# Optimization experiments

Hardware: AMD Instinct MI355X
Metric: run time of the kernel (lower is better)

## Reference

```python
import jax, jax.numpy as jnp
import numpy as np

B, T = 64, 2048
VOCAB, H, OUT = 32000, 256, 256


def setup_inputs() -> dict:
    key = jax.random.key(0)
    ks = jax.random.split(key, 6)
    x = jax.random.randint(ks[0], (B, T), 0, VOCAB, dtype=jnp.int32)
    embed = jax.random.normal(ks[1], (VOCAB, H), dtype=jnp.float32) * 0.02
    # torch Linear(h+h, h): weight [h, 2h]; we store transposed [2h, h]
    W_fc = jax.random.normal(ks[2], (2 * H, H), dtype=jnp.float32) * (1.0 / np.sqrt(2 * H))
    b_fc = jax.random.normal(ks[3], (H,), dtype=jnp.float32) * 0.01
    W_out = jax.random.normal(ks[4], (H, OUT), dtype=jnp.float32) * (1.0 / np.sqrt(H))
    b_out = jax.random.normal(ks[5], (OUT,), dtype=jnp.float32) * 0.01
    return {"x": x, "embed": embed, "W_fc": W_fc, "b_fc": b_fc, "W_out": W_out, "b_out": b_out}


def reference(x, embed, W_fc, b_fc, W_out, b_out):
    # SimpleRNN.forward_bptt: h_t = tanh(fc(concat([embed(x_t), h_{t-1}])))
    # concat-linear split: fc([e, h]) = e @ Wx + h @ Wh + b
    h_dim = embed.shape[1]
    Wx, Wh = W_fc[:h_dim], W_fc[h_dim:]
    xe = embed[x]                                   # [B, T, H] gather
    xproj = jnp.einsum('bth,hk->btk', xe, Wx) + b_fc  # precompute input projection

    def step(h, xp_t):
        h_new = jnp.tanh(xp_t + h @ Wh)
        return h_new, h_new

    h0 = jnp.zeros((x.shape[0], h_dim), dtype=embed.dtype)
    h_last, hs = jax.lax.scan(step, h0, jnp.swapaxes(xproj, 0, 1))  # hs: [T, B, H]
    hs = jnp.swapaxes(hs, 0, 1)                     # [B, T, H] = stack(hs[1:], dim=1)
    out = h_last @ W_out + b_out                    # [B, OUT]
    return out, hs
```

## Files before the change

kernel.cpp:

```cpp
#include <hip/hip_runtime.h>

#define RNN_T 2048
#define RNN_B 64
#define RNN_H 256
#define KBLK 36

typedef float v2f __attribute__((ext_vector_type(2)));

__global__ __launch_bounds__(256)
void xproj_kernel(const int* __restrict__ x, const float* __restrict__ embed,
                  const float* __restrict__ Wfc, const float* __restrict__ bfc,
                  float* __restrict__ hsb) {
    __shared__ int ixs[64];
    __shared__ __align__(16) float A[64][260];
    const int tid = threadIdx.x;
    const long rb0 = (long)blockIdx.x * 64;

    if (tid < 64) ixs[tid] = x[rb0 + tid];
    __syncthreads();

    {
        const int r = tid >> 2, q = tid & 3;
        const float* erow = embed + (long)ixs[r] * RNN_H;
        #pragma unroll
        for (int i = 0; i < 16; ++i) {
            const int c = q * 64 + i * 4;
            *(float4*)&A[r][c] = *(const float4*)(erow + c);
        }
    }
    __syncthreads();

    const int tj = tid & 31, tr = tid >> 5;
    const int r0 = tr * 8, j0 = tj * 4, j1 = 128 + tj * 4;

    float acc[8][8];
    #pragma unroll
    for (int i = 0; i < 8; ++i)
        #pragma unroll
        for (int c = 0; c < 8; ++c) acc[i][c] = 0.f;

    for (int k4 = 0; k4 < 64; ++k4) {
        float4 a[8];
        #pragma unroll
        for (int i = 0; i < 8; ++i) a[i] = *(const float4*)&A[r0 + i][k4 * 4];
        #pragma unroll
        for (int kk = 0; kk < 4; ++kk) {
            const int k = k4 * 4 + kk;
            const float4 wa = *(const float4*)(Wfc + (long)k * RNN_H + j0);
            const float4 wb = *(const float4*)(Wfc + (long)k * RNN_H + j1);
            #pragma unroll
            for (int i = 0; i < 8; ++i) {
                const float av = reinterpret_cast<const float*>(&a[i])[kk];
                acc[i][0] = fmaf(av, wa.x, acc[i][0]);
                acc[i][1] = fmaf(av, wa.y, acc[i][1]);
                acc[i][2] = fmaf(av, wa.z, acc[i][2]);
                acc[i][3] = fmaf(av, wa.w, acc[i][3]);
                acc[i][4] = fmaf(av, wb.x, acc[i][4]);
                acc[i][5] = fmaf(av, wb.y, acc[i][5]);
                acc[i][6] = fmaf(av, wb.z, acc[i][6]);
                acc[i][7] = fmaf(av, wb.w, acc[i][7]);
            }
        }
    }

    const float4 ba = *(const float4*)(bfc + j0);
    const float4 bb = *(const float4*)(bfc + j1);
    #pragma unroll
    for (int i = 0; i < 8; ++i) {
        const long row = rb0 + r0 + i;
        float4 o1 = make_float4(acc[i][0] + ba.x, acc[i][1] + ba.y,
                                acc[i][2] + ba.z, acc[i][3] + ba.w);
        float4 o2 = make_float4(acc[i][4] + bb.x, acc[i][5] + bb.y,
                                acc[i][6] + bb.z, acc[i][7] + bb.w);
        *(float4*)(hsb + row * RNN_H + j0) = o1;
        *(float4*)(hsb + row * RNN_H + j1) = o2;
    }
}

__device__ __forceinline__ float red8_dpp(float x) {
    int v = __float_as_int(x);
    x += __int_as_float(__builtin_amdgcn_update_dpp(0, v, 0xB1, 0xf, 0xf, true));
    v = __float_as_int(x);
    x += __int_as_float(__builtin_amdgcn_update_dpp(0, v, 0x4E, 0xf, 0xf, true));
    v = __float_as_int(x);
    x += __int_as_float(__builtin_amdgcn_update_dpp(0, v, 0x141, 0xf, 0xf, true));
    return x;
}

__device__ __forceinline__ v2f lo2(const float4 v) { return (v2f){v.x, v.y}; }
__device__ __forceinline__ v2f hi2(const float4 v) { return (v2f){v.z, v.w}; }

__global__ __launch_bounds__(512, 2)
void rnn_scan_kernel(const float* __restrict__ Wfc, const float* __restrict__ Wout,
                     const float* __restrict__ bout, float* __restrict__ out,
                     float* __restrict__ hsb) {
    __shared__ __align__(16) float hA[8 * KBLK];
    __shared__ __align__(16) float hB[8 * KBLK];
    const int tid = threadIdx.x;
    const int b = blockIdx.x;
    const int w = tid >> 6, l = tid & 63;
    const int cg = w * 8 + (l >> 3);
    const int kg = l & 7;
    const int c0 = cg * 4;
    const int k0 = kg * 32;

    const float* Wh = Wfc + RNN_H * RNN_H;
    v2f wv[4][16];
    #pragma unroll
    for (int m = 0; m < 16; ++m) {
        const long kb = (long)(k0 + 2 * m) * RNN_H;
        #pragma unroll
        for (int c = 0; c < 4; ++c) {
            v2f t;
            t.x = Wh[kb + c0 + c];
            t.y = Wh[kb + RNN_H + c0 + c];
            wv[c][m] = t;
        }
    }
    #pragma unroll
    for (int m = 0; m < 16; ++m)
        asm volatile("" : "+v"(wv[0][m]), "+v"(wv[1][m]), "+v"(wv[2][m]), "+v"(wv[3][m]));

    if (tid < 8 * KBLK) { hA[tid] = 0.f; }

    float* xpb = hsb + (long)b * RNN_T * RNN_H;
    const bool wr = (kg < 4);
    const int jcol = c0 + (kg & 3);
    const int widx = (jcol >> 5) * KBLK + (jcol & 31);
    float* xw = xpb + jcol;
    const float* xpf = xpb + jcol + 2 * RNN_H;
    const float* xend = xpb + (long)RNN_T * RNN_H;

    float xr = 0.f, xn = 0.f;
    if (wr) { xr = xpb[jcol]; xn = xpb[RNN_H + jcol]; }
    __syncthreads();

    const float4* rdA = (const float4*)(hA + kg * KBLK);
    const float4* rdB = (const float4*)(hB + kg * KBLK);

#define RNN_STEP(RD, WDST)                                                  \
    {                                                                       \
        float xf = 0.f;                                                     \
        if (wr && xpf < xend) xf = *xpf;                                    \
        xpf += RNN_H;                                                       \
        const float4 q0 = RD[0], q1 = RD[1], q2 = RD[2], q3 = RD[3];        \
        const float4 q4 = RD[4], q5 = RD[5], q6 = RD[6], q7 = RD[7];        \
        v2f a0 = {0.f,0.f}, a1 = {0.f,0.f}, a2 = {0.f,0.f}, a3 = {0.f,0.f}; \
        const v2f hp[16] = { lo2(q0), hi2(q0), lo2(q1), hi2(q1),            \
                             lo2(q2), hi2(q2), lo2(q3), hi2(q3),            \
                             lo2(q4), hi2(q4), lo2(q5), hi2(q5),            \
                             lo2(q6), hi2(q6), lo2(q7), hi2(q7) };          \
        _Pragma("unroll")                                                   \
        for (int m = 0; m < 16; ++m) {                                      \
            a0 = __builtin_elementwise_fma(hp[m], wv[0][m], a0);            \
            a1 = __builtin_elementwise_fma(hp[m], wv[1][m], a1);            \
            a2 = __builtin_elementwise_fma(hp[m], wv[2][m], a2);            \
            a3 = __builtin_elementwise_fma(hp[m], wv[3][m], a3);            \
        }                                                                   \
        const float r0 = red8_dpp(a0.x + a0.y);                             \
        const float r1 = red8_dpp(a1.x + a1.y);                             \
        const float r2 = red8_dpp(a2.x + a2.y);                             \
        const float r3 = red8_dpp(a3.x + a3.y);                             \
        if (wr) {                                                           \
            const float sv = (kg == 0) ? r0 : (kg == 1) ? r1                \
                           : (kg == 2) ? r2 : r3;                           \
            const float vsum = sv + xr;                                     \
            const float e = __expf(2.f * vsum);                             \
            const float hn = 1.f - 2.f * __builtin_amdgcn_rcpf(e + 1.f);    \
            WDST[widx] = hn;                                                \
            *xw = hn;                                                       \
            xr = xn; xn = xf;                                               \
        }                                                                   \
        xw += RNN_H;                                                        \
        __syncthreads();                                                    \
    }

    for (int t = 0; t < RNN_T; t += 2) {
        RNN_STEP(rdA, hB);
        RNN_STEP(rdB, hA);
    }
#undef RNN_STEP

    if (tid < RNN_H) {
        float a0 = 0.f, a1 = 0.f, a2 = 0.f, a3 = 0.f;
        for (int k = 0; k < RNN_H; k += 4) {
            const int kb = (k >> 5) * KBLK + (k & 31);
            a0 = fmaf(hA[kb + 0], Wout[(long)(k + 0) * RNN_H + tid], a0);
            a1 = fmaf(hA[kb + 1], Wout[(long)(k + 1) * RNN_H + tid], a1);
            a2 = fmaf(hA[kb + 2], Wout[(long)(k + 2) * RNN_H + tid], a2);
            a3 = fmaf(hA[kb + 3], Wout[(long)(k + 3) * RNN_H + tid], a3);
        }
        out[(long)b * RNN_H + tid] = a0 + a1 + a2 + a3 + bout[tid];
    }
}

extern "C" void kernel_launch(void* const* d_in, const int* in_sizes, int n_in,
                              void* d_out, int out_size, void* d_ws, size_t ws_size,
                              hipStream_t stream) {
    const int*   x     = (const int*)d_in[0];
    const float* embed = (const float*)d_in[1];
    const float* Wfc   = (const float*)d_in[2];
    const float* bfc   = (const float*)d_in[3];
    const float* Wout  = (const float*)d_in[4];
    const float* bout  = (const float*)d_in[5];

    float* out = (float*)d_out;
    float* hsb = out + RNN_B * RNN_H;

    xproj_kernel<<<(RNN_B * RNN_T) / 64, 256, 0, stream>>>(x, embed, Wfc, bfc, hsb);
    rnn_scan_kernel<<<RNN_B, 512, 0, stream>>>(Wfc, Wout, bout, out, hsb);
}
```

Before: 1.464 ms.

## Repartition recurrent matvec to 8 columns by 16 k-slices with butterfly DPP reduction

Each thread now owns 8 output columns over a 16-element k-slice instead of 4 columns over 32, so each step needs half as many LDS float4 reads per thread. The cross-lane reduction becomes a transpose-style butterfly: values are exchanged and halved at each DPP hop, so 16 lanes reduce 8 partial sums with fewer DPP ops than four independent full reductions. The shared-memory layout changes to 16 rows with a stride of 20 floats. This trades simpler logic for more select instructions and a trickier lane mapping that must be exactly right for correctness.

```diff
diff --git a/kernel.cpp b/kernel.cpp
--- a/kernel.cpp
+++ b/kernel.cpp
@@ -3,7 +3,7 @@
 #define RNN_T 2048
 #define RNN_B 64
 #define RNN_H 256
-#define KBLK 36
+#define KSTR 20
 
 typedef float v2f __attribute__((ext_vector_type(2)));
 
@@ -77,15 +77,9 @@
     }
 }
 
-__device__ __forceinline__ float red8_dpp(float x) {
-    int v = __float_as_int(x);
-    x += __int_as_float(__builtin_amdgcn_update_dpp(0, v, 0xB1, 0xf, 0xf, true));
-    v = __float_as_int(x);
-    x += __int_as_float(__builtin_amdgcn_update_dpp(0, v, 0x4E, 0xf, 0xf, true));
-    v = __float_as_int(x);
-    x += __int_as_float(__builtin_amdgcn_update_dpp(0, v, 0x141, 0xf, 0xf, true));
-    return x;
-}
+#define DPP_HOP(val, CTRL)                                                  \
+    __int_as_float(__builtin_amdgcn_update_dpp(                             \
+        0, __float_as_int(val), CTRL, 0xf, 0xf, true))
 
 __device__ __forceinline__ v2f lo2(const float4 v) { return (v2f){v.x, v.y}; }
 __device__ __forceinline__ v2f hi2(const float4 v) { return (v2f){v.z, v.w}; }
@@ -94,23 +88,23 @@
 void rnn_scan_kernel(const float* __restrict__ Wfc, const float* __restrict__ Wout,
                      const float* __restrict__ bout, float* __restrict__ out,
                      float* __restrict__ hsb) {
-    __shared__ __align__(16) float hA[8 * KBLK];
-    __shared__ __align__(16) float hB[8 * KBLK];
+    __shared__ __align__(16) float hA[16 * KSTR];
+    __shared__ __align__(16) float hB[16 * KSTR];
     const int tid = threadIdx.x;
     const int b = blockIdx.x;
     const int w = tid >> 6, l = tid & 63;
-    const int cg = w * 8 + (l >> 3);
-    const int kg = l & 7;
-    const int c0 = cg * 4;
-    const int k0 = kg * 32;
+    const int cg = w * 4 + (l >> 4);
+    const int s  = l & 15;
+    const int c0 = cg * 8;
+    const int k0 = s * 16;
 
     const float* Wh = Wfc + RNN_H * RNN_H;
-    v2f wv[4][16];
-    #pragma unroll
-    for (int m = 0; m < 16; ++m) {
+    v2f wv[8][8];
+    #pragma unroll
+    for (int m = 0; m < 8; ++m) {
         const long kb = (long)(k0 + 2 * m) * RNN_H;
         #pragma unroll
-        for (int c = 0; c < 4; ++c) {
+        for (int c = 0; c < 8; ++c) {
             v2f t;
             t.x = Wh[kb + c0 + c];
             t.y = Wh[kb + RNN_H + c0 + c];
@@ -118,15 +112,16 @@
         }
     }
     #pragma unroll
-    for (int m = 0; m < 16; ++m)
-        asm volatile("" : "+v"(wv[0][m]), "+v"(wv[1][m]), "+v"(wv[2][m]), "+v"(wv[3][m]));
-
-    if (tid < 8 * KBLK) { hA[tid] = 0.f; }
+    for (int m = 0; m < 8; ++m)
+        asm volatile("" : "+v"(wv[0][m]), "+v"(wv[1][m]), "+v"(wv[2][m]), "+v"(wv[3][m]),
+                          "+v"(wv[4][m]), "+v"(wv[5][m]), "+v"(wv[6][m]), "+v"(wv[7][m]));
+
+    if (tid < 16 * KSTR) hA[tid] = 0.f;
 
     float* xpb = hsb + (long)b * RNN_T * RNN_H;
-    const bool wr = (kg < 4);
-    const int jcol = c0 + (kg & 3);
-    const int widx = (jcol >> 5) * KBLK + (jcol & 31);
+    const bool wr = ((s & 4) == 0);
+    const int jcol = c0 + ((s & 3) | ((s & 8) ? 4 : 0));
+    const int widx = (jcol >> 4) * KSTR + (jcol & 15);
     float* xw = xpb + jcol;
     const float* xpf = xpb + jcol + 2 * RNN_H;
     const float* xend = xpb + (long)RNN_T * RNN_H;
@@ -135,8 +130,9 @@
     if (wr) { xr = xpb[jcol]; xn = xpb[RNN_H + jcol]; }
     __syncthreads();
 
-    const float4* rdA = (const float4*)(hA + kg * KBLK);
-    const float4* rdB = (const float4*)(hB + kg * KBLK);
+    const float4* rdA = (const float4*)(hA + s * KSTR);
+    const float4* rdB = (const float4*)(hB + s * KSTR);
+    const bool m1 = (l & 1), m2 = (l & 2), m8 = (l & 8);
 
 #define RNN_STEP(RD, WDST)                                                  \
     {                                                                       \
@@ -144,27 +140,37 @@
         if (wr && xpf < xend) xf = *xpf;                                    \
         xpf += RNN_H;                                                       \
         const float4 q0 = RD[0], q1 = RD[1], q2 = RD[2], q3 = RD[3];        \
-        const float4 q4 = RD[4], q5 = RD[5], q6 = RD[6], q7 = RD[7];        \
-        v2f a0 = {0.f,0.f}, a1 = {0.f,0.f}, a2 = {0.f,0.f}, a3 = {0.f,0.f}; \
-        const v2f hp[16] = { lo2(q0), hi2(q0), lo2(q1), hi2(q1),            \
-                             lo2(q2), hi2(q2), lo2(q3), hi2(q3),            \
-                             lo2(q4), hi2(q4), lo2(q5), hi2(q5),            \
-                             lo2(q6), hi2(q6), lo2(q7), hi2(q7) };          \
+        const v2f hp[8] = { lo2(q0), hi2(q0), lo2(q1), hi2(q1),             \
+                            lo2(q2), hi2(q2), lo2(q3), hi2(q3) };           \
+        v2f a0={0,0},a1={0,0},a2={0,0},a3={0,0},                            \
+            a4={0,0},a5={0,0},a6={0,0},a7={0,0};                            \
         _Pragma("unroll")                                                   \
-        for (int m = 0; m < 16; ++m) {                                      \
+        for (int m = 0; m < 8; ++m) {                                       \
             a0 = __builtin_elementwise_fma(hp[m], wv[0][m], a0);            \
             a1 = __builtin_elementwise_fma(hp[m], wv[1][m], a1);            \
             a2 = __builtin_elementwise_fma(hp[m], wv[2][m], a2);            \
             a3 = __builtin_elementwise_fma(hp[m], wv[3][m], a3);            \
+            a4 = __builtin_elementwise_fma(hp[m], wv[4][m], a4);            \
+            a5 = __builtin_elementwise_fma(hp[m], wv[5][m], a5);            \
+            a6 = __builtin_elementwise_fma(hp[m], wv[6][m], a6);            \
+            a7 = __builtin_elementwise_fma(hp[m], wv[7][m], a7);            \
         }                                                                   \
-        const float r0 = red8_dpp(a0.x + a0.y);                             \
-        const float r1 = red8_dpp(a1.x + a1.y);                             \
-        const float r2 = red8_dpp(a2.x + a2.y);                             \
-        const float r3 = red8_dpp(a3.x + a3.y);                             \
+        float s0=a0.x+a0.y, s1=a1.x+a1.y, s2=a2.x+a2.y, s3=a3.x+a3.y;       \
+        float s4=a4.x+a4.y, s5=a5.x+a5.y, s6=a6.x+a6.y, s7=a7.x+a7.y;       \
+                                \
+        float b0 = (m1 ? s1 : s0) + DPP_HOP(m1 ? s0 : s1, 0xB1);            \
+        float b1 = (m1 ? s3 : s2) + DPP_HOP(m1 ? s2 : s3, 0xB1);            \
+        float b2 = (m1 ? s5 : s4) + DPP_HOP(m1 ? s4 : s5, 0xB1);            \
+        float b3 = (m1 ? s7 : s6) + DPP_HOP(m1 ? s6 : s7, 0xB1);            \
+                                \
+        float c0v = (m2 ? b1 : b0) + DPP_HOP(m2 ? b0 : b1, 0x4E);           \
+        float c1v = (m2 ? b3 : b2) + DPP_HOP(m2 ? b2 : b3, 0x4E);           \
+                     \
+        float dv = (m8 ? c1v : c0v) + DPP_HOP(m8 ? c0v : c1v, 0x128);       \
+                    \
+        dv += DPP_HOP(DPP_HOP(dv, 0x1B), 0x141);                            \
         if (wr) {                                                           \
-            const float sv = (kg == 0) ? r0 : (kg == 1) ? r1                \
-                           : (kg == 2) ? r2 : r3;                           \
-            const float vsum = sv + xr;                                     \
+            const float vsum = dv + xr;                                     \
             const float e = __expf(2.f * vsum);                             \
             const float hn = 1.f - 2.f * __builtin_amdgcn_rcpf(e + 1.f);    \
             WDST[widx] = hn;                                                \
@@ -184,7 +190,7 @@
     if (tid < RNN_H) {
         float a0 = 0.f, a1 = 0.f, a2 = 0.f, a3 = 0.f;
         for (int k = 0; k < RNN_H; k += 4) {
-            const int kb = (k >> 5) * KBLK + (k & 31);
+            const int kb = (k >> 4) * KSTR + (k & 15);
             a0 = fmaf(hA[kb + 0], Wout[(long)(k + 0) * RNN_H + tid], a0);
             a1 = fmaf(hA[kb + 1], Wout[(long)(k + 1) * RNN_H + tid], a1);
             a2 = fmaf(hA[kb + 2], Wout[(long)(k + 2) * RNN_H + tid], a2);
```

Measured after the change: 1.329 ms. 1.1x faster.
